# Kernel optimization log

Measured on AMD Instinct MI355X. Metric: run time of the kernel, lower is better.

Reference implementation:

```python
import jax, jax.numpy as jnp
import numpy as np

N = 21  # nodes per graph (20 laser sectors + 1 robot node)
MAX_RANGE = 10.0
_bound = np.linspace(-np.pi / 2 - 0.03, np.pi / 2, 21, dtype=np.float32)[:-1]
_angles = _bound + np.float32(np.pi / 20)
ANGLE_FEAT = jnp.asarray(np.stack([np.sin(_angles), np.cos(_angles)], 1), dtype=jnp.float32)  # [20,2]


def _build_nodes(state24):
    # state24: [B,24] -> node features [B,21,7]
    B = state24.shape[0]
    laser = state24[:, :20, None] / MAX_RANGE                       # [B,20,1]
    angle = jnp.broadcast_to(ANGLE_FEAT[None], (B, 20, 2))          # [B,20,2]
    sector = jnp.concatenate([laser, angle, jnp.zeros((B, 20, 4), state24.dtype)], -1)  # [B,20,7]
    robot = jnp.concatenate([jnp.zeros((B, 1, 3), state24.dtype), state24[:, None, 20:]], -1)  # [B,1,7]
    return jnp.concatenate([sector, robot], axis=1)                 # [B,21,7]


def _gatv2(x, Wl, Wr, att, bias, heads, dim):
    # GATv2 over a fully-connected graph with self-loops (dense all-pairs).
    # e_ij = att . leaky_relu(Wl x_j + Wr x_i); alpha = softmax_j; out_i = sum_j alpha_ij (Wl x_j)
    B = x.shape[0]
    gl = (x @ Wl).reshape(B, N, heads, dim)  # source transform [B,j,H,D]
    gr = (x @ Wr).reshape(B, N, heads, dim)  # target transform [B,i,H,D]
    s = jax.nn.leaky_relu(gl[:, None] + gr[:, :, None], negative_slope=0.2)  # [B,i,j,H,D]
    e = jnp.einsum('bijhd,hd->bijh', s, att)                                  # [B,i,j,H]
    alpha = jax.nn.softmax(e, axis=2)                                          # softmax over sources j
    out = jnp.einsum('bijh,bjhd->bihd', alpha, gl).reshape(B, N, heads * dim)
    return out + bias


def setup_inputs() -> dict:
    key = jax.random.key(0)
    ks = jax.random.split(key, 16)
    r = lambda k, shape, s: (jax.random.normal(k, shape, dtype=jnp.float32) * s)
    B = 1024
    return {
        'state24': jax.random.normal(ks[0], (B, 24), dtype=jnp.float32),
        'Wl1': r(ks[1], (7, 256), 0.3), 'Wr1': r(ks[2], (7, 256), 0.3),
        'att1': r(ks[3], (4, 64), 0.1), 'b1': r(ks[4], (256,), 0.02),
        'Wl2': r(ks[5], (256, 64), 0.06), 'Wr2': r(ks[6], (256, 64), 0.06),
        'att2': r(ks[7], (1, 64), 0.1), 'b2': r(ks[8], (64,), 0.02),
        'fc1_w': r(ks[9], (64, 256), 0.12), 'fc1_b': r(ks[10], (256,), 0.02),
        'fc2_w': r(ks[11], (256, 256), 0.06), 'fc2_b': r(ks[12], (256,), 0.02),
        'fc3_w': r(ks[13], (256, 2), 0.06), 'fc3_b': r(ks[14], (2,), 0.02),
    }


def reference(state24, Wl1, Wr1, att1, b1, Wl2, Wr2, att2, b2,
              fc1_w, fc1_b, fc2_w, fc2_b, fc3_w, fc3_b):
    x = _build_nodes(state24)                               # [B,21,7]
    h = jax.nn.elu(_gatv2(x, Wl1, Wr1, att1, b1, 4, 64))    # [B,21,256]
    h = _gatv2(h, Wl2, Wr2, att2, b2, 1, 64)                # [B,21,64]
    nfv = jnp.mean(h, axis=1)                               # global_mean_pool -> [B,64]
    h = jax.nn.relu(nfv @ fc1_w + fc1_b)
    h = jax.nn.relu(h @ fc2_w + fc2_b)
    return jnp.tanh(h @ fc3_w + fc3_b)                      # [B,2]
```

## Files before the change

kernel.cpp:

```cpp
#include <hip/hip_runtime.h>
#include <hip/hip_fp16.h>
#include <math.h>

#define PI_D 3.141592653589793

typedef _Float16 h2 __attribute__((ext_vector_type(2)));
typedef _Float16 h4 __attribute__((ext_vector_type(4)));
typedef _Float16 h8 __attribute__((ext_vector_type(8)));
typedef unsigned short us8 __attribute__((ext_vector_type(8)));
typedef __fp16 f16v2 __attribute__((ext_vector_type(2)));
typedef __fp16 f16v8 __attribute__((ext_vector_type(8)));
typedef float f32x4 __attribute__((ext_vector_type(4)));

#define STR1 264
#define STR2H 72

#define SV(v, a, b) __builtin_shufflevector(v, v, a, b)

static __device__ __forceinline__ h2 pack_h2(float a, float b) {
    return __builtin_bit_cast(h2, __builtin_amdgcn_cvt_pkrtz(a, b));
}

static __device__ __forceinline__ float fdot2(h2 a, h2 b, float c) {
    return __builtin_amdgcn_fdot2(__builtin_bit_cast(f16v2, a),
                                  __builtin_bit_cast(f16v2, b), c, false);
}

static __device__ __forceinline__ h8 habs8(h8 x) {
    us8 u = __builtin_bit_cast(us8, x);
    us8 m = {0x7fff, 0x7fff, 0x7fff, 0x7fff, 0x7fff, 0x7fff, 0x7fff, 0x7fff};
    return __builtin_bit_cast(h8, (us8)(u & m));
}

static __device__ __forceinline__ f32x4 mfma16(h8 a, h8 b, f32x4 c) {
    return __builtin_amdgcn_mfma_f32_16x16x32_f16(
        __builtin_bit_cast(f16v8, a), __builtin_bit_cast(f16v8, b), c, 0, 0, 0);
}

static __device__ __forceinline__ void wave_fence() {
    asm volatile("" ::: "memory");
#if __has_builtin(__builtin_amdgcn_wave_barrier)
    __builtin_amdgcn_wave_barrier();
#endif
    asm volatile("" ::: "memory");
}

__global__ __launch_bounds__(256, 4) void actor_fused_kernel(
    const float* __restrict__ state24,
    const float* __restrict__ Wl1, const float* __restrict__ Wr1,
    const float* __restrict__ att1, const float* __restrict__ b1,
    const float* __restrict__ Wl2, const float* __restrict__ Wr2,
    const float* __restrict__ att2, const float* __restrict__ b2,
    const float* __restrict__ fc1_w, const float* __restrict__ fc1_b,
    const float* __restrict__ fc2_w, const float* __restrict__ fc2_b,
    const float* __restrict__ fc3_w, const float* __restrict__ fc3_b,
    float* __restrict__ out, int B)
{
    const int smp = blockIdx.x;
    const int tid = threadIdx.x;

    __shared__ float sinL[20], cosL[20], laserL[20], robotL[4];
    __shared__ __align__(16) h2 attLh[128];
    __shared__ __align__(16) h2 att2Lh[32];
    __shared__ __align__(16) _Float16 gr1h[22 * STR1];
    __shared__ __align__(16) union {
        struct { _Float16 gl1h[22 * STR1];
                 float ePf[128 * 24];
                 float uv[168]; } p1;
        struct { _Float16 gl2h[21 * STR2H];
                 _Float16 gr2h[21 * STR2H];
                 _Float16 gl2hT[64 * 32];
                 float e2[32 * 24];
                 float u2v2[42];
                 float red[4][256];
                 _Float16 nfvh[64]; _Float16 hah[256]; _Float16 hbh[256]; } p2;
    } U;

    if (tid < 20) {
        double step = (PI_D + 0.03) / 20.0;
        float bound = (float)(-PI_D / 2.0 - 0.03 + (double)tid * step);
        float ang = bound + (float)(PI_D / 20.0);
        sinL[tid] = sinf(ang);
        cosL[tid] = cosf(ang);
        laserL[tid] = state24[smp * 24 + tid] * 0.1f;
    }
    if (tid >= 32 && tid < 36) {
        int q = tid - 32;
        robotL[q] = state24[smp * 24 + 20 + q];
    }
    if (tid < 128) {
        float2 ap = ((const float2*)att1)[tid];
        attLh[tid] = pack_h2(0.4f * ap.x, 0.4f * ap.y);
    }
    if (tid >= 128 && tid < 160) {
        float2 ap = ((const float2*)att2)[tid - 128];
        att2Lh[tid - 128] = pack_h2(0.4f * ap.x, 0.4f * ap.y);
    }
    __syncthreads();

    {
        const int h = tid >> 6;
        const int lane = tid & 63;

        {
            const int cp = lane & 31;
            const int half = lane >> 5;
            const int d2 = h * 32 + cp;
            float2 wl[7], wr[7];
            #pragma unroll
            for (int k = 0; k < 7; k++) {
                wl[k] = ((const float2*)Wl1)[k * 128 + d2];
                wr[k] = ((const float2*)Wr1)[k * 128 + d2];
            }
            if (half == 0) {
                h2 zz2 = {};
                ((h2*)(U.p1.gl1h + 21 * STR1))[d2] = zz2;
                ((h2*)(gr1h + 21 * STR1))[d2] = zz2;
            }
            const int base = half * 11;
            #pragma unroll
            for (int nn = 0; nn < 11; ++nn) {
                int node = base + nn;
                if (node < 21) {
                    float a0, a1, b0, b1v;
                    if (node < 20) {
                        float l = laserL[node], sv = sinL[node], c = cosL[node];
                        a0 = l * wl[0].x + sv * wl[1].x + c * wl[2].x;
                        a1 = l * wl[0].y + sv * wl[1].y + c * wl[2].y;
                        b0 = l * wr[0].x + sv * wr[1].x + c * wr[2].x;
                        b1v = l * wr[0].y + sv * wr[1].y + c * wr[2].y;
                    } else {
                        float r0 = robotL[0], r1 = robotL[1], r2 = robotL[2], r3 = robotL[3];
                        a0 = r0 * wl[3].x + r1 * wl[4].x + r2 * wl[5].x + r3 * wl[6].x;
                        a1 = r0 * wl[3].y + r1 * wl[4].y + r2 * wl[5].y + r3 * wl[6].y;
                        b0 = r0 * wr[3].x + r1 * wr[4].x + r2 * wr[5].x + r3 * wr[6].x;
                        b1v = r0 * wr[3].y + r1 * wr[4].y + r2 * wr[5].y + r3 * wr[6].y;
                    }
                    ((h2*)(U.p1.gl1h + node * STR1))[d2] = pack_h2(a0, a1);
                    ((h2*)(gr1h + node * STR1))[d2] = pack_h2(b0, b1v);
                }
            }
        }
        wave_fence();

        {
            h2 ar[32];
            #pragma unroll
            for (int q = 0; q < 32; ++q) ar[q] = attLh[h * 32 + q];

            const bool act = lane < 63;
            const int jn  = act ? lane % 21 : 0;
            const int seg = act ? lane / 21 : 0;

            const h8* gA8 = (const h8*)(U.p1.gl1h + jn * STR1 + h * 64);
            h8 gj[8];
            #pragma unroll
            for (int ch = 0; ch < 8; ++ch) gj[ch] = gA8[ch];

            if (act && seg == 0) {
                float l0 = 0.f, l1 = 0.f;
                #pragma unroll
                for (int ch = 0; ch < 8; ++ch) {
                    l0 = fdot2(SV(gj[ch], 0, 1), ar[ch * 4 + 0], l0);
                    l1 = fdot2(SV(gj[ch], 2, 3), ar[ch * 4 + 1], l1);
                    l0 = fdot2(SV(gj[ch], 4, 5), ar[ch * 4 + 2], l0);
                    l1 = fdot2(SV(gj[ch], 6, 7), ar[ch * 4 + 3], l1);
                }
                U.p1.uv[h * 21 + jn] = l0 + l1;
            }

            #pragma unroll
            for (int t = 0; t < 7; ++t) {
                const int i = seg * 7 + t;
                const h8* gB8 = (const h8*)(gr1h + i * STR1 + h * 64);
                float m0 = 0.f, m1 = 0.f;
                #pragma unroll
                for (int ch = 0; ch < 8; ++ch) {
                    h8 x = gj[ch] + gB8[ch];
                    h8 ax = habs8(x);
                    m0 = fdot2(SV(ax, 0, 1), ar[ch * 4 + 0], m0);
                    m1 = fdot2(SV(ax, 2, 3), ar[ch * 4 + 1], m1);
                    m0 = fdot2(SV(ax, 4, 5), ar[ch * 4 + 2], m0);
                    m1 = fdot2(SV(ax, 6, 7), ar[ch * 4 + 3], m1);
                }
                if (act) U.p1.ePf[(h * 32 + i) * 24 + jn] = m0 + m1;
            }

            if (lane < 21) {
                const h8* row8 = (const h8*)(gr1h + lane * STR1 + h * 64);
                float l0 = 0.f, l1 = 0.f;
                #pragma unroll
                for (int ch = 0; ch < 8; ++ch) {
                    h8 g = row8[ch];
                    l0 = fdot2(SV(g, 0, 1), ar[ch * 4 + 0], l0);
                    l1 = fdot2(SV(g, 2, 3), ar[ch * 4 + 1], l1);
                    l0 = fdot2(SV(g, 4, 5), ar[ch * 4 + 2], l0);
                    l1 = fdot2(SV(g, 6, 7), ar[ch * 4 + 3], l1);
                }
                U.p1.uv[84 + h * 21 + lane] = l0 + l1;
            }
        }
        wave_fence();

        if (lane < 21) {
            int i = lane;
            int r = h * 32 + i;
            float* row = U.p1.ePf + r * 24;
            const float* uu = U.p1.uv + h * 21;
            float vi = 1.5f * U.p1.uv[84 + h * 21 + i];
            float ebuf[21];
            float m = -1e30f;
            #pragma unroll
            for (int j = 0; j < 21; j++) {
                float e = row[j] + 1.5f * uu[j] + vi;
                ebuf[j] = e;
                m = fmaxf(m, e);
            }
            float sum = 0.f;
            #pragma unroll
            for (int j = 0; j < 21; j++) { float v = __expf(ebuf[j] - m); ebuf[j] = v; sum += v; }
            float rinv = 1.f / sum;
            h8* hp8 = (h8*)(U.p1.ePf) + r * 6;
            h8 o0, o1, o2;
            #pragma unroll
            for (int q = 0; q < 8; ++q) o0[q] = (_Float16)(ebuf[q] * rinv);
            #pragma unroll
            for (int q = 0; q < 8; ++q) o1[q] = (_Float16)(ebuf[8 + q] * rinv);
            #pragma unroll
            for (int q = 0; q < 5; ++q) o2[q] = (_Float16)(ebuf[16 + q] * rinv);
            o2[5] = (_Float16)0.f; o2[6] = (_Float16)0.f; o2[7] = (_Float16)0.f;
            h8 zz = {};
            hp8[0] = o0; hp8[1] = o1; hp8[2] = o2;
            hp8[3] = zz; hp8[4] = zz; hp8[5] = zz;
        }
        {
            h8 zz = {};
            for (int z = lane; z < 66; z += 64) {
                int rr = z / 6, slot = z - rr * 6;
                ((h8*)U.p1.ePf)[(h * 32 + 21 + rr) * 6 + slot] = zz;
            }
        }
        wave_fence();

        {
            const int mcol = lane & 15;
            const int quad = lane >> 4;
            const h8* Af = (const h8*)U.p1.ePf;
            h8 A0 = Af[(h * 32 + mcol) * 6 + quad];
            h8 A1 = Af[(h * 32 + 16 + mcol) * 6 + quad];
            int rowoff[8];
            #pragma unroll
            for (int jj = 0; jj < 8; ++jj) {
                int rr = quad * 8 + jj;
                rowoff[jj] = (rr > 21 ? 21 : rr) * STR1;
            }
            const int colbase = h * 64 + mcol;
            f32x4 z4 = {0.f, 0.f, 0.f, 0.f};
            #pragma unroll
            for (int t = 0; t < 4; ++t) {
                int col = colbase + t * 16;
                float bb = b1[col];
                h8 bv;
                #pragma unroll
                for (int jj = 0; jj < 8; ++jj) bv[jj] = U.p1.gl1h[rowoff[jj] + col];
                f32x4 d0 = mfma16(A0, bv, z4);
                f32x4 d1 = mfma16(A1, bv, z4);
                #pragma unroll
                for (int r = 0; r < 4; ++r) {
                    int n0 = quad * 4 + r;
                    float v = d0[r] + bb;
                    v = v > 0.f ? v : __expf(v) - 1.f;
                    gr1h[n0 * STR1 + col] = (_Float16)v;
                    int n1 = 16 + quad * 4 + r;
                    if (n1 < 21) {
                        float w2 = d1[r] + bb;
                        w2 = w2 > 0.f ? w2 : __expf(w2) - 1.f;
                        gr1h[n1 * STR1 + col] = (_Float16)w2;
                    }
                }
            }
        }
    }
    __syncthreads();

    {
        const int lane = tid & 63;
        const int w = tid >> 6;
        const int mrow = lane & 15;
        const int quad = lane >> 4;
        int rowA1 = 16 + mrow; if (rowA1 > 21) rowA1 = 21;
        const int ncol = w * 16 + mrow;
        const float* pL = Wl2 + ncol;
        const float* pR = Wr2 + ncol;
        f32x4 aL0 = {0.f, 0.f, 0.f, 0.f}, aL1 = {0.f, 0.f, 0.f, 0.f};
        f32x4 aR0 = {0.f, 0.f, 0.f, 0.f}, aR1 = {0.f, 0.f, 0.f, 0.f};
        #pragma unroll
        for (int kc = 0; kc < 8; ++kc) {
            const int kb = kc * 32 + quad * 8;
            h8 BL, BR;
            #pragma unroll
            for (int j = 0; j < 8; ++j) {
                BL[j] = (_Float16)pL[(kb + j) * 64];
                BR[j] = (_Float16)pR[(kb + j) * 64];
            }
            h8 A0 = *(const h8*)(gr1h + mrow * STR1 + quad * 8 + kc * 32);
            h8 A1 = *(const h8*)(gr1h + rowA1 * STR1 + quad * 8 + kc * 32);
            aL0 = mfma16(A0, BL, aL0);
            aL1 = mfma16(A1, BL, aL1);
            aR0 = mfma16(A0, BR, aR0);
            aR1 = mfma16(A1, BR, aR1);
        }
        const int col = ncol;
        #pragma unroll
        for (int r = 0; r < 4; ++r) {
            int row0 = quad * 4 + r;
            U.p2.gl2h[row0 * STR2H + col] = (_Float16)aL0[r];
            U.p2.gr2h[row0 * STR2H + col] = (_Float16)aR0[r];
            int row1 = 16 + row0;
            if (row1 < 21) {
                U.p2.gl2h[row1 * STR2H + col] = (_Float16)aL1[r];
                U.p2.gr2h[row1 * STR2H + col] = (_Float16)aR1[r];
            }
        }
        h2 lo0 = pack_h2(aL0[0], aL0[1]);
        h2 hi0 = pack_h2(aL0[2], aL0[3]);
        h4 p0 = __builtin_shufflevector(lo0, hi0, 0, 1, 2, 3);
        *(h4*)(U.p2.gl2hT + col * 32 + quad * 4) = p0;
        h2 lo1 = pack_h2(aL1[0], aL1[1]);
        h2 hi1 = pack_h2(aL1[2], aL1[3]);
        h4 p1 = __builtin_shufflevector(lo1, hi1, 0, 1, 2, 3);
        *(h4*)(U.p2.gl2hT + col * 32 + 16 + quad * 4) = p1;
    }
    __syncthreads();

    {
        h2 ar2[32];
        #pragma unroll
        for (int q = 0; q < 32; ++q) ar2[q] = att2Lh[q];

        const bool act = tid < 252;
        const int t0 = act ? tid : 0;
        const int jn = t0 % 21;
        const int sg = t0 / 21;

        const h8* gA8 = (const h8*)(U.p2.gl2h + jn * STR2H);
        h8 gj[8];
        #pragma unroll
        for (int ch = 0; ch < 8; ++ch) gj[ch] = gA8[ch];

        if (act && sg == 0) {
            float l0 = 0.f, l1 = 0.f;
            #pragma unroll
            for (int ch = 0; ch < 8; ++ch) {
                l0 = fdot2(SV(gj[ch], 0, 1), ar2[ch * 4 + 0], l0);
                l1 = fdot2(SV(gj[ch], 2, 3), ar2[ch * 4 + 1], l1);
                l0 = fdot2(SV(gj[ch], 4, 5), ar2[ch * 4 + 2], l0);
                l1 = fdot2(SV(gj[ch], 6, 7), ar2[ch * 4 + 3], l1);
            }
            U.p2.u2v2[jn] = l0 + l1;
        }

        if (sg < 11) {
            #pragma unroll
            for (int tt = 0; tt < 2; ++tt) {
                const int i = sg * 2 + tt;
                const int ri = i < 21 ? i : 20;
                const h8* gB8 = (const h8*)(U.p2.gr2h + ri * STR2H);
                float m0 = 0.f, m1 = 0.f;
                #pragma unroll
                for (int ch = 0; ch < 8; ++ch) {
                    h8 x = gj[ch] + gB8[ch];
                    h8 ax = habs8(x);
                    m0 = fdot2(SV(ax, 0, 1), ar2[ch * 4 + 0], m0);
                    m1 = fdot2(SV(ax, 2, 3), ar2[ch * 4 + 1], m1);
                    m0 = fdot2(SV(ax, 4, 5), ar2[ch * 4 + 2], m0);
                    m1 = fdot2(SV(ax, 6, 7), ar2[ch * 4 + 3], m1);
                }
                if (act && i < 21) U.p2.e2[i * 24 + jn] = m0 + m1;
            }
        } else if (act) {
            const h8* row8 = (const h8*)(U.p2.gr2h + jn * STR2H);
            float l0 = 0.f, l1 = 0.f;
            #pragma unroll
            for (int ch = 0; ch < 8; ++ch) {
                h8 g = row8[ch];
                l0 = fdot2(SV(g, 0, 1), ar2[ch * 4 + 0], l0);
                l1 = fdot2(SV(g, 2, 3), ar2[ch * 4 + 1], l1);
                l0 = fdot2(SV(g, 4, 5), ar2[ch * 4 + 2], l0);
                l1 = fdot2(SV(g, 6, 7), ar2[ch * 4 + 3], l1);
            }
            U.p2.u2v2[21 + jn] = l0 + l1;
        }
    }
    __syncthreads();

    if (tid < 21) {
        int i = tid;
        float* row = U.p2.e2 + i * 24;
        const float* uu = U.p2.u2v2;
        float vi = 1.5f * U.p2.u2v2[21 + i];
        float ebuf[21];
        float m = -1e30f;
        #pragma unroll
        for (int j = 0; j < 21; j++) {
            float e = row[j] + 1.5f * uu[j] + vi;
            ebuf[j] = e;
            m = fmaxf(m, e);
        }
        float sum = 0.f;
        #pragma unroll
        for (int j = 0; j < 21; j++) { float v = __expf(ebuf[j] - m); ebuf[j] = v; sum += v; }
        float rinv = 1.f / sum;
        h8* hp8 = (h8*)(U.p2.e2) + i * 6;
        h8 o0, o1, o2;
        #pragma unroll
        for (int q = 0; q < 8; ++q) o0[q] = (_Float16)(ebuf[q] * rinv);
        #pragma unroll
        for (int q = 0; q < 8; ++q) o1[q] = (_Float16)(ebuf[8 + q] * rinv);
        #pragma unroll
        for (int q = 0; q < 5; ++q) o2[q] = (_Float16)(ebuf[16 + q] * rinv);
        o2[5] = (_Float16)0.f; o2[6] = (_Float16)0.f; o2[7] = (_Float16)0.f;
        h8 zz = {};
        hp8[0] = o0; hp8[1] = o1; hp8[2] = o2;
        hp8[3] = zz; hp8[4] = zz; hp8[5] = zz;
    } else if (tid < 87) {
        int z = tid - 21;
        int rr = z / 6, slot = z - rr * 6;
        h8 zz = {};
        ((h8*)U.p2.e2)[(21 + rr) * 6 + slot] = zz;
    }
    __syncthreads();

    {
        const int lane = tid & 63;
        const int w = tid >> 6;
        const int mcol = lane & 15;
        const int quad = lane >> 4;
        const int col = w * 16 + mcol;
        float bb = b2[col];
        f32x4 z4 = {0.f, 0.f, 0.f, 0.f};
        const h8* Af2 = (const h8*)U.p2.e2;
        h8 A0 = Af2[mcol * 6 + quad];
        h8 A1 = Af2[(16 + mcol) * 6 + quad];
        h8 bv = *(const h8*)(U.p2.gl2hT + col * 32 + quad * 8);
        f32x4 d0 = mfma16(A0, bv, z4);
        f32x4 d1 = mfma16(A1, bv, z4);
        float sum = (d0[0] + d0[1]) + (d0[2] + d0[3])
                  + (d1[0] + d1[1]) + (d1[2] + d1[3]);
        sum += __shfl_xor(sum, 16, 64);
        sum += __shfl_xor(sum, 32, 64);
        if (quad == 0) U.p2.nfvh[col] = (_Float16)(sum * (1.f / 21.f) + bb);
    }
    __syncthreads();

    {
        int c = tid & 63, g = tid >> 6;
        const float4* W1 = (const float4*)fc1_w;
        float4 acc = {0.f, 0.f, 0.f, 0.f};
        #pragma unroll
        for (int kk = 0; kk < 8; ++kk) {
            int k2 = g * 8 + kk;
            float4 r0 = W1[(2 * k2) * 64 + c];
            float4 r1 = W1[(2 * k2 + 1) * 64 + c];
            h2 x = ((const h2*)U.p2.nfvh)[k2];
            float x0 = (float)x[0], x1 = (float)x[1];
            acc.x = fmaf(r0.x, x0, fmaf(r1.x, x1, acc.x));
            acc.y = fmaf(r0.y, x0, fmaf(r1.y, x1, acc.y));
            acc.z = fmaf(r0.z, x0, fmaf(r1.z, x1, acc.z));
            acc.w = fmaf(r0.w, x0, fmaf(r1.w, x1, acc.w));
        }
        ((float4*)U.p2.red[g])[c] = acc;
    }
    __syncthreads();
    {
        float bb = fc1_b[tid];
        float v = U.p2.red[0][tid] + U.p2.red[1][tid]
                + U.p2.red[2][tid] + U.p2.red[3][tid] + bb;
        U.p2.hah[tid] = (_Float16)fmaxf(v, 0.f);
    }
    __syncthreads();

    {
        int c = tid & 63, g = tid >> 6;
        const float4* W2 = (const float4*)fc2_w;
        const h8* ha = (const h8*)U.p2.hah;
        float4 acc = {0.f, 0.f, 0.f, 0.f};
        #pragma unroll
        for (int q = 0; q < 8; ++q) {
            h8 xa = ha[g * 8 + q];
            #pragma unroll
            for (int p = 0; p < 4; ++p) {
                int k2 = g * 32 + q * 4 + p;
                float4 r0 = W2[(2 * k2) * 64 + c];
                float4 r1 = W2[(2 * k2 + 1) * 64 + c];
                float x0 = (float)xa[2 * p], x1 = (float)xa[2 * p + 1];
                acc.x = fmaf(r0.x, x0, fmaf(r1.x, x1, acc.x));
                acc.y = fmaf(r0.y, x0, fmaf(r1.y, x1, acc.y));
                acc.z = fmaf(r0.z, x0, fmaf(r1.z, x1, acc.z));
                acc.w = fmaf(r0.w, x0, fmaf(r1.w, x1, acc.w));
            }
        }
        ((float4*)U.p2.red[g])[c] = acc;
    }
    __syncthreads();
    {
        float bb = fc2_b[tid];
        float v = U.p2.red[0][tid] + U.p2.red[1][tid]
                + U.p2.red[2][tid] + U.p2.red[3][tid] + bb;
        U.p2.hbh[tid] = (_Float16)fmaxf(v, 0.f);
    }
    __syncthreads();

    {
        int g = tid >> 6;
        if (g < 2) {
            int o = g;
            int l = tid & 63;
            float sum = 0.f;
            #pragma unroll
            for (int m = 0; m < 4; m++) {
                int k = l + 64 * m;
                sum = fmaf((float)U.p2.hbh[k], fc3_w[k * 2 + o], sum);
            }
            #pragma unroll
            for (int off = 32; off >= 1; off >>= 1) sum += __shfl_down(sum, off, 64);
            if (l == 0) out[smp * 2 + o] = tanhf(sum + fc3_b[o]);
        }
    }
}

extern "C" void kernel_launch(void* const* d_in, const int* in_sizes, int n_in,
                              void* d_out, int out_size, void* d_ws, size_t ws_size,
                              hipStream_t stream) {
    const float* state24 = (const float*)d_in[0];
    const float* Wl1 = (const float*)d_in[1];
    const float* Wr1 = (const float*)d_in[2];
    const float* att1 = (const float*)d_in[3];
    const float* b1 = (const float*)d_in[4];
    const float* Wl2 = (const float*)d_in[5];
    const float* Wr2 = (const float*)d_in[6];
    const float* att2 = (const float*)d_in[7];
    const float* b2 = (const float*)d_in[8];
    const float* fc1_w = (const float*)d_in[9];
    const float* fc1_b = (const float*)d_in[10];
    const float* fc2_w = (const float*)d_in[11];
    const float* fc2_b = (const float*)d_in[12];
    const float* fc3_w = (const float*)d_in[13];
    const float* fc3_b = (const float*)d_in[14];
    float* out = (float*)d_out;

    (void)d_ws; (void)ws_size;

    int B = in_sizes[0] / 24;
    actor_fused_kernel<<<B, 256, 0, stream>>>(
        state24, Wl1, Wr1, att1, b1, Wl2, Wr2, att2, b2,
        fc1_w, fc1_b, fc2_w, fc2_b, fc3_w, fc3_b, out, B);
}
```

Baseline: 115.6 us.

## Double block size to 512 threads and redistribute GAT stages across eight waves

Result: slower. 218.1 us (+88.7%).

```diff
diff --git a/kernel.cpp b/kernel.cpp
--- a/kernel.cpp
+++ b/kernel.cpp
@@ -37,15 +37,7 @@
         __builtin_bit_cast(f16v8, a), __builtin_bit_cast(f16v8, b), c, 0, 0, 0);
 }
 
-static __device__ __forceinline__ void wave_fence() {
-    asm volatile("" ::: "memory");
-#if __has_builtin(__builtin_amdgcn_wave_barrier)
-    __builtin_amdgcn_wave_barrier();
-#endif
-    asm volatile("" ::: "memory");
-}
-
-__global__ __launch_bounds__(256, 4) void actor_fused_kernel(
+__global__ __launch_bounds__(512, 8) void actor_fused_kernel(
     const float* __restrict__ state24,
     const float* __restrict__ Wl1, const float* __restrict__ Wr1,
     const float* __restrict__ att1, const float* __restrict__ b1,
@@ -58,6 +50,8 @@
 {
     const int smp = blockIdx.x;
     const int tid = threadIdx.x;
+    const int wid = tid >> 6;
+    const int lane = tid & 63;
 
     __shared__ float sinL[20], cosL[20], laserL[20], robotL[4];
     __shared__ __align__(16) h2 attLh[128];
@@ -72,7 +66,7 @@
                  _Float16 gl2hT[64 * 32];
                  float e2[32 * 24];
                  float u2v2[42];
-                 float red[4][256];
+                 float red[8][256];
                  _Float16 nfvh[64]; _Float16 hah[256]; _Float16 hbh[256]; } p2;
     } U;
 
@@ -99,79 +93,77 @@
     __syncthreads();
 
     {
-        const int h = tid >> 6;
-        const int lane = tid & 63;
-
-        {
-            const int cp = lane & 31;
-            const int half = lane >> 5;
-            const int d2 = h * 32 + cp;
-            float2 wl[7], wr[7];
-            #pragma unroll
-            for (int k = 0; k < 7; k++) {
-                wl[k] = ((const float2*)Wl1)[k * 128 + d2];
-                wr[k] = ((const float2*)Wr1)[k * 128 + d2];
-            }
-            if (half == 0) {
-                h2 zz2 = {};
-                ((h2*)(U.p1.gl1h + 21 * STR1))[d2] = zz2;
-                ((h2*)(gr1h + 21 * STR1))[d2] = zz2;
-            }
-            const int base = half * 11;
-            #pragma unroll
-            for (int nn = 0; nn < 11; ++nn) {
-                int node = base + nn;
-                if (node < 21) {
-                    float a0, a1, b0, b1v;
-                    if (node < 20) {
-                        float l = laserL[node], sv = sinL[node], c = cosL[node];
-                        a0 = l * wl[0].x + sv * wl[1].x + c * wl[2].x;
-                        a1 = l * wl[0].y + sv * wl[1].y + c * wl[2].y;
-                        b0 = l * wr[0].x + sv * wr[1].x + c * wr[2].x;
-                        b1v = l * wr[0].y + sv * wr[1].y + c * wr[2].y;
-                    } else {
-                        float r0 = robotL[0], r1 = robotL[1], r2 = robotL[2], r3 = robotL[3];
-                        a0 = r0 * wl[3].x + r1 * wl[4].x + r2 * wl[5].x + r3 * wl[6].x;
-                        a1 = r0 * wl[3].y + r1 * wl[4].y + r2 * wl[5].y + r3 * wl[6].y;
-                        b0 = r0 * wr[3].x + r1 * wr[4].x + r2 * wr[5].x + r3 * wr[6].x;
-                        b1v = r0 * wr[3].y + r1 * wr[4].y + r2 * wr[5].y + r3 * wr[6].y;
-                    }
-                    ((h2*)(U.p1.gl1h + node * STR1))[d2] = pack_h2(a0, a1);
-                    ((h2*)(gr1h + node * STR1))[d2] = pack_h2(b0, b1v);
+        const int d2 = tid & 127;
+        const int qtr = tid >> 7;
+        float2 wl[7], wr[7];
+        #pragma unroll
+        for (int k = 0; k < 7; k++) {
+            wl[k] = ((const float2*)Wl1)[k * 128 + d2];
+            wr[k] = ((const float2*)Wr1)[k * 128 + d2];
+        }
+        if (qtr == 0) {
+            h2 zz2 = {};
+            ((h2*)(U.p1.gl1h + 21 * STR1))[d2] = zz2;
+            ((h2*)(gr1h + 21 * STR1))[d2] = zz2;
+        }
+        const int base = qtr * 6;
+        #pragma unroll
+        for (int nn = 0; nn < 6; ++nn) {
+            int node = base + nn;
+            if (node < 21) {
+                float a0, a1, b0, b1v;
+                if (node < 20) {
+                    float l = laserL[node], sv = sinL[node], c = cosL[node];
+                    a0 = l * wl[0].x + sv * wl[1].x + c * wl[2].x;
+                    a1 = l * wl[0].y + sv * wl[1].y + c * wl[2].y;
+                    b0 = l * wr[0].x + sv * wr[1].x + c * wr[2].x;
+                    b1v = l * wr[0].y + sv * wr[1].y + c * wr[2].y;
+                } else {
+                    float r0 = robotL[0], r1 = robotL[1], r2 = robotL[2], r3 = robotL[3];
+                    a0 = r0 * wl[3].x + r1 * wl[4].x + r2 * wl[5].x + r3 * wl[6].x;
+                    a1 = r0 * wl[3].y + r1 * wl[4].y + r2 * wl[5].y + r3 * wl[6].y;
+                    b0 = r0 * wr[3].x + r1 * wr[4].x + r2 * wr[5].x + r3 * wr[6].x;
+                    b1v = r0 * wr[3].y + r1 * wr[4].y + r2 * wr[5].y + r3 * wr[6].y;
                 }
-            }
-        }
-        wave_fence();
-
-        {
-            h2 ar[32];
-            #pragma unroll
-            for (int q = 0; q < 32; ++q) ar[q] = attLh[h * 32 + q];
-
-            const bool act = lane < 63;
-            const int jn  = act ? lane % 21 : 0;
-            const int seg = act ? lane / 21 : 0;
-
-            const h8* gA8 = (const h8*)(U.p1.gl1h + jn * STR1 + h * 64);
-            h8 gj[8];
-            #pragma unroll
-            for (int ch = 0; ch < 8; ++ch) gj[ch] = gA8[ch];
-
-            if (act && seg == 0) {
-                float l0 = 0.f, l1 = 0.f;
-                #pragma unroll
-                for (int ch = 0; ch < 8; ++ch) {
-                    l0 = fdot2(SV(gj[ch], 0, 1), ar[ch * 4 + 0], l0);
-                    l1 = fdot2(SV(gj[ch], 2, 3), ar[ch * 4 + 1], l1);
-                    l0 = fdot2(SV(gj[ch], 4, 5), ar[ch * 4 + 2], l0);
-                    l1 = fdot2(SV(gj[ch], 6, 7), ar[ch * 4 + 3], l1);
-                }
-                U.p1.uv[h * 21 + jn] = l0 + l1;
-            }
-
-            #pragma unroll
-            for (int t = 0; t < 7; ++t) {
-                const int i = seg * 7 + t;
+                ((h2*)(U.p1.gl1h + node * STR1))[d2] = pack_h2(a0, a1);
+                ((h2*)(gr1h + node * STR1))[d2] = pack_h2(b0, b1v);
+            }
+        }
+    }
+    __syncthreads();
+
+    {
+        const int h = wid >> 1;
+        const int p = (wid & 1) * 64 + lane;
+        h2 ar[32];
+        #pragma unroll
+        for (int q = 0; q < 32; ++q) ar[q] = attLh[h * 32 + q];
+
+        const bool act = p < 126;
+        const int jn  = act ? p % 21 : 0;
+        const int seg = act ? p / 21 : 0;
+
+        const h8* gA8 = (const h8*)(U.p1.gl1h + jn * STR1 + h * 64);
+        h8 gj[8];
+        #pragma unroll
+        for (int ch = 0; ch < 8; ++ch) gj[ch] = gA8[ch];
+
+        if (act && seg == 0) {
+            float l0 = 0.f, l1 = 0.f;
+            #pragma unroll
+            for (int ch = 0; ch < 8; ++ch) {
+                l0 = fdot2(SV(gj[ch], 0, 1), ar[ch * 4 + 0], l0);
+                l1 = fdot2(SV(gj[ch], 2, 3), ar[ch * 4 + 1], l1);
+                l0 = fdot2(SV(gj[ch], 4, 5), ar[ch * 4 + 2], l0);
+                l1 = fdot2(SV(gj[ch], 6, 7), ar[ch * 4 + 3], l1);
+            }
+            U.p1.uv[h * 21 + jn] = l0 + l1;
+        }
+
+        #pragma unroll
+        for (int t = 0; t < 4; ++t) {
+            const int i = seg * 4 + t;
+            if (i < 21) {
                 const h8* gB8 = (const h8*)(gr1h + i * STR1 + h * 64);
                 float m0 = 0.f, m1 = 0.f;
                 #pragma unroll
@@ -185,25 +177,30 @@
                 }
                 if (act) U.p1.ePf[(h * 32 + i) * 24 + jn] = m0 + m1;
             }
-
-            if (lane < 21) {
-                const h8* row8 = (const h8*)(gr1h + lane * STR1 + h * 64);
-                float l0 = 0.f, l1 = 0.f;
-                #pragma unroll
-                for (int ch = 0; ch < 8; ++ch) {
-                    h8 g = row8[ch];
-                    l0 = fdot2(SV(g, 0, 1), ar[ch * 4 + 0], l0);
-                    l1 = fdot2(SV(g, 2, 3), ar[ch * 4 + 1], l1);
-                    l0 = fdot2(SV(g, 4, 5), ar[ch * 4 + 2], l0);
-                    l1 = fdot2(SV(g, 6, 7), ar[ch * 4 + 3], l1);
-                }
-                U.p1.uv[84 + h * 21 + lane] = l0 + l1;
-            }
-        }
-        wave_fence();
-
-        if (lane < 21) {
-            int i = lane;
+        }
+
+        if (p >= 21 && p < 42) {
+            const int idx = p - 21;
+            const h8* row8 = (const h8*)(gr1h + idx * STR1 + h * 64);
+            float l0 = 0.f, l1 = 0.f;
+            #pragma unroll
+            for (int ch = 0; ch < 8; ++ch) {
+                h8 g = row8[ch];
+                l0 = fdot2(SV(g, 0, 1), ar[ch * 4 + 0], l0);
+                l1 = fdot2(SV(g, 2, 3), ar[ch * 4 + 1], l1);
+                l0 = fdot2(SV(g, 4, 5), ar[ch * 4 + 2], l0);
+                l1 = fdot2(SV(g, 6, 7), ar[ch * 4 + 3], l1);
+            }
+            U.p1.uv[84 + h * 21 + idx] = l0 + l1;
+        }
+    }
+    __syncthreads();
+
+    {
+        const int h = wid >> 1;
+        const int sub = wid & 1;
+        if (lane < 11 - sub) {
+            int i = sub * 11 + lane;
             int r = h * 32 + i;
             float* row = U.p1.ePf + r * 24;
             const float* uu = U.p1.uv + h * 21;
@@ -234,49 +231,46 @@
             hp8[3] = zz; hp8[4] = zz; hp8[5] = zz;
         }
         {
-            h8 zz = {};
-            for (int z = lane; z < 66; z += 64) {
+            int z = sub * 64 + lane;
+            if (z < 66) {
                 int rr = z / 6, slot = z - rr * 6;
+                h8 zz = {};
                 ((h8*)U.p1.ePf)[(h * 32 + 21 + rr) * 6 + slot] = zz;
             }
         }
-        wave_fence();
-
-        {
-            const int mcol = lane & 15;
-            const int quad = lane >> 4;
-            const h8* Af = (const h8*)U.p1.ePf;
-            h8 A0 = Af[(h * 32 + mcol) * 6 + quad];
-            h8 A1 = Af[(h * 32 + 16 + mcol) * 6 + quad];
-            int rowoff[8];
-            #pragma unroll
-            for (int jj = 0; jj < 8; ++jj) {
-                int rr = quad * 8 + jj;
-                rowoff[jj] = (rr > 21 ? 21 : rr) * STR1;
-            }
-            const int colbase = h * 64 + mcol;
-            f32x4 z4 = {0.f, 0.f, 0.f, 0.f};
-            #pragma unroll
-            for (int t = 0; t < 4; ++t) {
-                int col = colbase + t * 16;
-                float bb = b1[col];
-                h8 bv;
-                #pragma unroll
-                for (int jj = 0; jj < 8; ++jj) bv[jj] = U.p1.gl1h[rowoff[jj] + col];
-                f32x4 d0 = mfma16(A0, bv, z4);
-                f32x4 d1 = mfma16(A1, bv, z4);
-                #pragma unroll
-                for (int r = 0; r < 4; ++r) {
-                    int n0 = quad * 4 + r;
-                    float v = d0[r] + bb;
+    }
+    __syncthreads();
+
+    {
+        const int h = wid >> 1;
+        const int sub = wid & 1;
+        const int mcol = lane & 15;
+        const int quad = lane >> 4;
+        const h8* Af = (const h8*)U.p1.ePf;
+        h8 A = Af[(h * 32 + sub * 16 + mcol) * 6 + quad];
+        int rowoff[8];
+        #pragma unroll
+        for (int jj = 0; jj < 8; ++jj) {
+            int rr = quad * 8 + jj;
+            rowoff[jj] = (rr > 21 ? 21 : rr) * STR1;
+        }
+        const int colbase = h * 64 + mcol;
+        f32x4 z4 = {0.f, 0.f, 0.f, 0.f};
+        #pragma unroll
+        for (int t = 0; t < 4; ++t) {
+            int col = colbase + t * 16;
+            float bb = b1[col];
+            h8 bv;
+            #pragma unroll
+            for (int jj = 0; jj < 8; ++jj) bv[jj] = U.p1.gl1h[rowoff[jj] + col];
+            f32x4 d = mfma16(A, bv, z4);
+            #pragma unroll
+            for (int r = 0; r < 4; ++r) {
+                int n = sub * 16 + quad * 4 + r;
+                if (n < 21) {
+                    float v = d[r] + bb;
                     v = v > 0.f ? v : __expf(v) - 1.f;
-                    gr1h[n0 * STR1 + col] = (_Float16)v;
-                    int n1 = 16 + quad * 4 + r;
-                    if (n1 < 21) {
-                        float w2 = d1[r] + bb;
-                        w2 = w2 > 0.f ? w2 : __expf(w2) - 1.f;
-                        gr1h[n1 * STR1 + col] = (_Float16)w2;
-                    }
+                    gr1h[n * STR1 + col] = (_Float16)v;
                 }
             }
         }
@@ -284,16 +278,15 @@
     __syncthreads();
 
     {
-        const int lane = tid & 63;
-        const int w = tid >> 6;
+        const int ntile = wid >> 1;
+        const int rhalf = wid & 1;
         const int mrow = lane & 15;
         const int quad = lane >> 4;
-        int rowA1 = 16 + mrow; if (rowA1 > 21) rowA1 = 21;
-        const int ncol = w * 16 + mrow;
+        int arow = rhalf ? (16 + mrow > 21 ? 21 : 16 + mrow) : mrow;
+        const int ncol = ntile * 16 + mrow;
         const float* pL = Wl2 + ncol;
         const float* pR = Wr2 + ncol;
-        f32x4 aL0 = {0.f, 0.f, 0.f, 0.f}, aL1 = {0.f, 0.f, 0.f, 0.f};
-        f32x4 aR0 = {0.f, 0.f, 0.f, 0.f}, aR1 = {0.f, 0.f, 0.f, 0.f};
+        f32x4 aL = {0.f, 0.f, 0.f, 0.f}, aR = {0.f, 0.f, 0.f, 0.f};
         #pragma unroll
         for (int kc = 0; kc < 8; ++kc) {
             const int kb = kc * 32 + quad * 8;
@@ -303,33 +296,23 @@
                 BL[j] = (_Float16)pL[(kb + j) * 64];
                 BR[j] = (_Float16)pR[(kb + j) * 64];
             }
-            h8 A0 = *(const h8*)(gr1h + mrow * STR1 + quad * 8 + kc * 32);
-            h8 A1 = *(const h8*)(gr1h + rowA1 * STR1 + quad * 8 + kc * 32);
-            aL0 = mfma16(A0, BL, aL0);
-            aL1 = mfma16(A1, BL, aL1);
-            aR0 = mfma16(A0, BR, aR0);
-            aR1 = mfma16(A1, BR, aR1);
+            h8 A = *(const h8*)(gr1h + arow * STR1 + quad * 8 + kc * 32);
+            aL = mfma16(A, BL, aL);
+            aR = mfma16(A, BR, aR);
         }
         const int col = ncol;
         #pragma unroll
         for (int r = 0; r < 4; ++r) {
-            int row0 = quad * 4 + r;
-            U.p2.gl2h[row0 * STR2H + col] = (_Float16)aL0[r];
-            U.p2.gr2h[row0 * STR2H + col] = (_Float16)aR0[r];
-            int row1 = 16 + row0;
-            if (row1 < 21) {
-                U.p2.gl2h[row1 * STR2H + col] = (_Float16)aL1[r];
-                U.p2.gr2h[row1 * STR2H + col] = (_Float16)aR1[r];
-            }
-        }
-        h2 lo0 = pack_h2(aL0[0], aL0[1]);
-        h2 hi0 = pack_h2(aL0[2], aL0[3]);
-        h4 p0 = __builtin_shufflevector(lo0, hi0, 0, 1, 2, 3);
-        *(h4*)(U.p2.gl2hT + col * 32 + quad * 4) = p0;
-        h2 lo1 = pack_h2(aL1[0], aL1[1]);
-        h2 hi1 = pack_h2(aL1[2], aL1[3]);
-        h4 p1 = __builtin_shufflevector(lo1, hi1, 0, 1, 2, 3);
-        *(h4*)(U.p2.gl2hT + col * 32 + 16 + quad * 4) = p1;
+            int row = rhalf * 16 + quad * 4 + r;
+            if (row < 21) {
+                U.p2.gl2h[row * STR2H + col] = (_Float16)aL[r];
+                U.p2.gr2h[row * STR2H + col] = (_Float16)aR[r];
+            }
+        }
+        h2 lo = pack_h2(aL[0], aL[1]);
+        h2 hi = pack_h2(aL[2], aL[3]);
+        h4 pq = __builtin_shufflevector(lo, hi, 0, 1, 2, 3);
+        *(h4*)(U.p2.gl2hT + col * 32 + rhalf * 16 + quad * 4) = pq;
     }
     __syncthreads();
 
@@ -338,48 +321,27 @@
         #pragma unroll
         for (int q = 0; q < 32; ++q) ar2[q] = att2Lh[q];
 
-        const bool act = tid < 252;
-        const int t0 = act ? tid : 0;
-        const int jn = t0 % 21;
-        const int sg = t0 / 21;
-
-        const h8* gA8 = (const h8*)(U.p2.gl2h + jn * STR2H);
-        h8 gj[8];
-        #pragma unroll
-        for (int ch = 0; ch < 8; ++ch) gj[ch] = gA8[ch];
-
-        if (act && sg == 0) {
-            float l0 = 0.f, l1 = 0.f;
+        const int p = tid;
+        if (p < 441) {
+            const int i = p / 21;
+            const int jn = p - i * 21;
+            const h8* gA8 = (const h8*)(U.p2.gl2h + jn * STR2H);
+            const h8* gB8 = (const h8*)(U.p2.gr2h + i * STR2H);
+            float m0 = 0.f, m1 = 0.f;
             #pragma unroll
             for (int ch = 0; ch < 8; ++ch) {
-                l0 = fdot2(SV(gj[ch], 0, 1), ar2[ch * 4 + 0], l0);
-                l1 = fdot2(SV(gj[ch], 2, 3), ar2[ch * 4 + 1], l1);
-                l0 = fdot2(SV(gj[ch], 4, 5), ar2[ch * 4 + 2], l0);
-                l1 = fdot2(SV(gj[ch], 6, 7), ar2[ch * 4 + 3], l1);
-            }
-            U.p2.u2v2[jn] = l0 + l1;
-        }
-
-        if (sg < 11) {
-            #pragma unroll
-            for (int tt = 0; tt < 2; ++tt) {
-                const int i = sg * 2 + tt;
-                const int ri = i < 21 ? i : 20;
-                const h8* gB8 = (const h8*)(U.p2.gr2h + ri * STR2H);
-                float m0 = 0.f, m1 = 0.f;
-                #pragma unroll
-                for (int ch = 0; ch < 8; ++ch) {
-                    h8 x = gj[ch] + gB8[ch];
-                    h8 ax = habs8(x);
-                    m0 = fdot2(SV(ax, 0, 1), ar2[ch * 4 + 0], m0);
-                    m1 = fdot2(SV(ax, 2, 3), ar2[ch * 4 + 1], m1);
-                    m0 = fdot2(SV(ax, 4, 5), ar2[ch * 4 + 2], m0);
-                    m1 = fdot2(SV(ax, 6, 7), ar2[ch * 4 + 3], m1);
-                }
-                if (act && i < 21) U.p2.e2[i * 24 + jn] = m0 + m1;
-            }
-        } else if (act) {
-            const h8* row8 = (const h8*)(U.p2.gr2h + jn * STR2H);
+                h8 x = gA8[ch] + gB8[ch];
+                h8 ax = habs8(x);
+                m0 = fdot2(SV(ax, 0, 1), ar2[ch * 4 + 0], m0);
+                m1 = fdot2(SV(ax, 2, 3), ar2[ch * 4 + 1], m1);
+                m0 = fdot2(SV(ax, 4, 5), ar2[ch * 4 + 2], m0);
+                m1 = fdot2(SV(ax, 6, 7), ar2[ch * 4 + 3], m1);
+            }
+            U.p2.e2[i * 24 + jn] = m0 + m1;
+        } else if (p < 483) {
+            const int isV = p >= 462;
+            const int j = p - (isV ? 462 : 441);
+            const h8* row8 = (const h8*)((isV ? U.p2.gr2h : U.p2.gl2h) + j * STR2H);
             float l0 = 0.f, l1 = 0.f;
             #pragma unroll
             for (int ch = 0; ch < 8; ++ch) {
@@ -389,7 +351,7 @@
                 l0 = fdot2(SV(g, 4, 5), ar2[ch * 4 + 2], l0);
                 l1 = fdot2(SV(g, 6, 7), ar2[ch * 4 + 3], l1);
             }
-            U.p2.u2v2[21 + jn] = l0 + l1;
+            U.p2.u2v2[isV * 21 + j] = l0 + l1;
         }
     }
     __syncthreads();
@@ -431,12 +393,10 @@
     }
     __syncthreads();
 
-    {
-        const int lane = tid & 63;
-        const int w = tid >> 6;
+    if (wid < 4) {
         const int mcol = lane & 15;
         const int quad = lane >> 4;
-        const int col = w * 16 + mcol;
+        const int col = wid * 16 + mcol;
         float bb = b2[col];
         f32x4 z4 = {0.f, 0.f, 0.f, 0.f};
         const h8* Af2 = (const h8*)U.p2.e2;
@@ -458,8 +418,8 @@
         const float4* W1 = (const float4*)fc1_w;
         float4 acc = {0.f, 0.f, 0.f, 0.f};
         #pragma unroll
-        for (int kk = 0; kk < 8; ++kk) {
-            int k2 = g * 8 + kk;
+        for (int kk = 0; kk < 4; ++kk) {
+            int k2 = g * 4 + kk;
             float4 r0 = W1[(2 * k2) * 64 + c];
             float4 r1 = W1[(2 * k2 + 1) * 64 + c];
             h2 x = ((const h2*)U.p2.nfvh)[k2];
@@ -472,10 +432,10 @@
         ((float4*)U.p2.red[g])[c] = acc;
     }
     __syncthreads();
-    {
-        float bb = fc1_b[tid];
-        float v = U.p2.red[0][tid] + U.p2.red[1][tid]
-                + U.p2.red[2][tid] + U.p2.red[3][tid] + bb;
+    if (tid < 256) {
+        float v = fc1_b[tid];
+        #pragma unroll
+        for (int g = 0; g < 8; ++g) v += U.p2.red[g][tid];
         U.p2.hah[tid] = (_Float16)fmaxf(v, 0.f);
     }
     __syncthreads();
@@ -486,14 +446,14 @@
         const h8* ha = (const h8*)U.p2.hah;
         float4 acc = {0.f, 0.f, 0.f, 0.f};
         #pragma unroll
-        for (int q = 0; q < 8; ++q) {
-            h8 xa = ha[g * 8 + q];
-            #pragma unroll
-            for (int p = 0; p < 4; ++p) {
-                int k2 = g * 32 + q * 4 + p;
+        for (int q = 0; q < 4; ++q) {
+            h8 xa = ha[g * 4 + q];
+            #pragma unroll
+            for (int pp = 0; pp < 4; ++pp) {
+                int k2 = g * 16 + q * 4 + pp;
                 float4 r0 = W2[(2 * k2) * 64 + c];
                 float4 r1 = W2[(2 * k2 + 1) * 64 + c];
-                float x0 = (float)xa[2 * p], x1 = (float)xa[2 * p + 1];
+                float x0 = (float)xa[2 * pp], x1 = (float)xa[2 * pp + 1];
                 acc.x = fmaf(r0.x, x0, fmaf(r1.x, x1, acc.x));
                 acc.y = fmaf(r0.y, x0, fmaf(r1.y, x1, acc.y));
                 acc.z = fmaf(r0.z, x0, fmaf(r1.z, x1, acc.z));
@@ -503,10 +463,10 @@
         ((float4*)U.p2.red[g])[c] = acc;
     }
     __syncthreads();
-    {
-        float bb = fc2_b[tid];
-        float v = U.p2.red[0][tid] + U.p2.red[1][tid]
-                + U.p2.red[2][tid] + U.p2.red[3][tid] + bb;
+    if (tid < 256) {
+        float v = fc2_b[tid];
+        #pragma unroll
+        for (int g = 0; g < 8; ++g) v += U.p2.red[g][tid];
         U.p2.hbh[tid] = (_Float16)fmaxf(v, 0.f);
     }
     __syncthreads();
@@ -552,7 +512,7 @@
     (void)d_ws; (void)ws_size;
 
     int B = in_sizes[0] / 24;
-    actor_fused_kernel<<<B, 256, 0, stream>>>(
+    actor_fused_kernel<<<B, 512, 0, stream>>>(
         state24, Wl1, Wr1, att1, b1, Wl2, Wr2, att2, b2,
         fc1_w, fc1_b, fc2_w, fc2_b, fc3_w, fc3_b, out, B);
 }
```
